# Optimization experiments

Hardware: AMD Instinct MI355X
Metric: run time of the kernel (lower is better)

## Reference

```python
import jax, jax.numpy as jnp
import numpy as np

L, B, CIN, COUT, E, S = 4, 4, 64, 64, 512, 2048
EPS = 1e-6


def setup_inputs() -> dict:
    key = jax.random.key(0)
    ks = jax.random.split(key, 12)
    r = lambda k, shape: (jax.random.normal(k, shape, jnp.float32) * 0.02)
    return {
        'x': jax.random.normal(ks[0], (B, CIN, S), jnp.float32),
        'in_W': r(ks[1], (E, CIN)), 'in_b': jnp.zeros((E,), jnp.float32),
        'cc_W': r(ks[2], (E, E, 3)), 'cc_b': jnp.zeros((E,), jnp.float32),
        'ln1_g': jnp.ones((L, E), jnp.float32), 'ln1_b': jnp.zeros((L, E), jnp.float32),
        'ln2_g': jnp.ones((L, E), jnp.float32), 'ln2_b': jnp.zeros((L, E), jnp.float32),
        'Wq': r(ks[3], (L, E, E)), 'bq': jnp.zeros((L, E), jnp.float32),
        'Wk': r(ks[4], (L, E, E)), 'bk': jnp.zeros((L, E), jnp.float32),
        'Wv': r(ks[5], (L, E, E)), 'bv': jnp.zeros((L, E), jnp.float32),
        'Wo': r(ks[6], (L, E, E)), 'bo': jnp.zeros((L, E), jnp.float32),
        'c1_W': r(ks[7], (L, E, E)), 'c1_b': jnp.zeros((L, E), jnp.float32),
        'c2_W': r(ks[8], (L, E, E)), 'c2_b': jnp.zeros((L, E), jnp.float32),
        'out_W': r(ks[9], (COUT, E)), 'out_b': jnp.zeros((COUT,), jnp.float32),
    }


def _ln(x, g, b):
    m = jnp.mean(x, axis=-1, keepdims=True)
    v = jnp.var(x, axis=-1, keepdims=True)
    return (x - m) * jax.lax.rsqrt(v + 1e-5) * g + b


def _phi(z):
    return jax.nn.elu(z) + 1.0  # linear-attention feature map


def _lin_causal_attn(h, Wq, bq, Wk, bk, Wv, bv, Wo, bo):
    # h: [B, S, E]; causal linear attention in exact masked-quadratic form
    q = _phi(h @ Wq.T + bq)
    k = _phi(h @ Wk.T + bk)
    v = h @ Wv.T + bv
    scores = jnp.einsum('bse,bte->bst', q, k)  # [B, S, S]
    s = h.shape[1]
    mask = jnp.tril(jnp.ones((s, s), bool))
    scores = jnp.where(mask[None], scores, 0.0)
    num = jnp.einsum('bst,bte->bse', scores, v)
    den = jnp.sum(scores, axis=-1, keepdims=True)
    return (num / (den + EPS)) @ Wo.T + bo


def _causal_conv(z, W, b):
    # z: [B, E, S], W: [E, E, 3]; left-pad kernel-1 for causality
    y = jax.lax.conv_general_dilated(z, W, (1,), [(2, 0)],
                                     dimension_numbers=('NCH', 'OIH', 'NCH'))
    return y + b[None, :, None]


def _forward(x, in_W, in_b, cc_W, cc_b, ln1_g, ln1_b, ln2_g, ln2_b,
             Wq, bq, Wk, bk, Wv, bv, Wo, bo, c1_W, c1_b, c2_W, c2_b,
             out_W, out_b):
    lat = jnp.einsum('bcs,ec->bes', x, in_W) + in_b[None, :, None]  # input_layer (k=1 conv)
    lat = _causal_conv(lat, cc_W, cc_b)
    lat = lat.transpose(0, 2, 1)  # [B, S, E]
    for i in range(Wq.shape[0]):
        h = _ln(lat, ln1_g[i], ln1_b[i])
        lat = lat + _lin_causal_attn(h, Wq[i], bq[i], Wk[i], bk[i],
                                     Wv[i], bv[i], Wo[i], bo[i])
        h = _ln(lat, ln2_g[i], ln2_b[i])
        h = jax.nn.gelu(h @ c1_W[i].T + c1_b[i], approximate=False) @ c2_W[i].T + c2_b[i]
        lat = lat + h
    return jnp.einsum('bse,oe->bos', lat, out_W) + out_b[None, :, None]


def reference(x, in_W, in_b, cc_W, cc_b, ln1_g, ln1_b, ln2_g, ln2_b,
              Wq, bq, Wk, bk, Wv, bv, Wo, bo, c1_W, c1_b, c2_W, c2_b,
              out_W, out_b):
    return _forward(x, in_W, in_b, cc_W, cc_b, ln1_g, ln1_b, ln2_g, ln2_b,
                    Wq, bq, Wk, bk, Wv, bv, Wo, bo, c1_W, c1_b, c2_W, c2_b,
                    out_W, out_b)
```

## Files before the change

### kernel.cpp

```cpp
#include <hip/hip_runtime.h>
#include <hip/hip_bf16.h>
#include <cmath>

#define S_LEN 2048
#define E_DIM 512
#define B_SZ 4
#define CIN_D 64
#define COUT_D 64
#define L_NUM 4
#define CHK 256
#define NCHK 8
#define ROWS (B_SZ * S_LEN)
#define PADR 2050
#define QLD 1024

typedef __attribute__((ext_vector_type(8))) short short8;
typedef __attribute__((ext_vector_type(4))) float f32x4;
typedef unsigned short ushort_t;

__device__ __forceinline__ ushort_t f2b(float v) {
  __hip_bfloat16 t = __float2bfloat16(v);
  return __builtin_bit_cast(ushort_t, t);
}
__device__ __forceinline__ float b2f(ushort_t u) {
  return __builtin_bit_cast(float, ((unsigned)u) << 16);
}
__device__ __forceinline__ float b2f(unsigned u) {
  return __builtin_bit_cast(float, u << 16);
}

__device__ __forceinline__ void gload16(const void* g, void* l) {
  __builtin_amdgcn_global_load_lds((const __attribute__((address_space(1))) void*)g,
                                   (__attribute__((address_space(3))) void*)l, 16, 0, 0);
}

__device__ __forceinline__ void barrier_mem() {
  asm volatile("s_barrier" ::: "memory");
}
template <int N>
__device__ __forceinline__ void waitn() {
  if constexpr (N == 0) asm volatile("s_waitcnt vmcnt(0)" ::: "memory");
  else if constexpr (N == 6) asm volatile("s_waitcnt vmcnt(6)" ::: "memory");
  else asm volatile("s_waitcnt vmcnt(8)" ::: "memory");
  __builtin_amdgcn_sched_barrier(0);
}

struct GemmP {
  const ushort_t* A; const ushort_t* B; const float* bias;
  ushort_t* Cb; const float* den;
  int nkt, lda, ldb, ldc;
  int aZrow, aZcol, bZrow, bZcol, cZrow;
  const ushort_t* A2; const ushort_t* B2;
  int nkt2, lda2, ldb2, a2Zrow, b2Zrow;
};

template <int TM, int TN, bool CONV>
__device__ __forceinline__ void mma_phase(const ushort_t* A, const ushort_t* B,
                                          int nkt, int lda, int ldb, int arow0,
                                          int acol0, int brow0, int bcol0,
                                          char* sm, int tid,
                                          f32x4 (&acc)[TM / 32][TN / 32]) {
  constexpr int MF = TM / 32, NF = TN / 32;
  constexpr int ABY = TM * 128, BBY = TN * 128, BUF = ABY + BBY;
  constexpr int RA = ABY / 4096, RB = BBY / 4096;
  const int lane = tid & 63, w = tid >> 6;
  const int wr = (w >> 1) * (TM / 2), wc = (w & 1) * (TN / 2);
  const int l15 = lane & 15, l4 = lane >> 4;

  auto stage = [&](int kt, int buf) {
    int ar0 = arow0, ac0 = acol0 + (kt << 6);
    if (CONV) {
      ar0 = arow0 + (kt >> 3);
      ac0 = acol0 + ((kt & 7) << 6);
    }
    char* s = sm + buf * BUF;
#pragma unroll
    for (int r = 0; r < RA; ++r) {
      const int f = (r << 12) + (tid << 4);
      const int row = f >> 7, sw = ((((f >> 4) & 7)) ^ (row & 7)) << 3;
      gload16(A + (size_t)(ar0 + row) * lda + ac0 + sw, s + f);
    }
    const int bc0 = bcol0 + (kt << 6);
#pragma unroll
    for (int r = 0; r < RB; ++r) {
      const int f = (r << 12) + (tid << 4);
      const int row = f >> 7, sw = ((((f >> 4) & 7)) ^ (row & 7)) << 3;
      gload16(B + (size_t)(brow0 + row) * ldb + bc0 + sw, s + ABY + f);
    }
  };

  stage(0, 0);
  int cur = 0;
  for (int kt = 0; kt < nkt; ++kt) {
    if (kt + 1 < nkt) {
      stage(kt + 1, cur ^ 1);
      waitn<RA + RB>();
    } else {
      waitn<0>();
    }
    barrier_mem();
    char* s = sm + cur * BUF;
#pragma unroll
    for (int kk = 0; kk < 2; ++kk) {
      short8 af[MF], bfv[NF];
#pragma unroll
      for (int m = 0; m < MF; ++m) {
        const int rt = wr + (m << 4) + l15;
        af[m] = *(const short8*)(s + rt * 128 +
                                 (((kk << 6) + (l4 << 4)) ^ ((rt & 7) << 4)));
      }
#pragma unroll
      for (int n = 0; n < NF; ++n) {
        const int rt = wc + (n << 4) + l15;
        bfv[n] = *(const short8*)(s + ABY + rt * 128 +
                                  (((kk << 6) + (l4 << 4)) ^ ((rt & 7) << 4)));
      }
#pragma unroll
      for (int m = 0; m < MF; ++m)
#pragma unroll
        for (int n = 0; n < NF; ++n)
          acc[m][n] = __builtin_amdgcn_mfma_f32_16x16x32_bf16(af[m], bfv[n],
                                                              acc[m][n], 0, 0, 0);
    }
    __builtin_amdgcn_sched_barrier(0);
    asm volatile("s_waitcnt lgkmcnt(0)" ::: "memory");
    barrier_mem();
    cur ^= 1;
  }
}

template <int TM, int TN, int ACT, bool READC, bool PADA, bool PADC,
          bool BIASROW, bool TRIMASK, bool SKIPUP, bool DIVDEN, bool TWOPH,
          bool CONV, bool HALFK>
__device__ __forceinline__ void gemm_body(const GemmP& p, int bm, int bn,
                                          int z, int tid, char* smem) {
  constexpr int MF = TM / 32, NF = TN / 32;
  const int lane = tid & 63, w = tid >> 6;
  const int wr = (w >> 1) * (TM / 2), wc = (w & 1) * (TN / 2);
  const int l15 = lane & 15, l4 = lane >> 4;

  if (SKIPUP && bn >= bm + TM) {
#pragma unroll
    for (int m = 0; m < MF; ++m)
#pragma unroll
      for (int j = 0; j < 4; ++j) {
        const int rloc = bm + wr + (m << 4) + (l4 << 2) + j;
        const size_t crow = (size_t)p.cZrow * z + rloc;
#pragma unroll
        for (int n = 0; n < NF; ++n)
          p.Cb[crow * p.ldc + bn + wc + (n << 4) + l15] = 0;
      }
    return;
  }

  f32x4 acc[MF][NF];
#pragma unroll
  for (int m = 0; m < MF; ++m)
#pragma unroll
    for (int n = 0; n < NF; ++n)
#pragma unroll
      for (int j = 0; j < 4; ++j) acc[m][n][j] = 0.f;

  int arow0 = bm + p.aZrow * z;
  if (PADA) arow0 = bm + ((bm >> 11) << 1);
  int nkt1 = p.nkt;
  if (HALFK) nkt1 = min(p.nkt, (bm + TM) >> 6);
  mma_phase<TM, TN, CONV>(p.A, p.B, nkt1, p.lda, p.ldb, arow0, p.aZcol * z,
                          bn + p.bZrow * z, p.bZcol * z, smem, tid, acc);
  if (TWOPH)
    mma_phase<TM, TN, false>(p.A2, p.B2, p.nkt2, p.lda2, p.ldb2,
                             bm + p.a2Zrow * z, 0, bn + p.b2Zrow * z, 0, smem,
                             tid, acc);

  float bcol[NF];
  if (p.bias && !BIASROW) {
#pragma unroll
    for (int n = 0; n < NF; ++n) bcol[n] = p.bias[bn + wc + (n << 4) + l15];
  }
  int crow_base = bm;
  if (PADC) crow_base = bm + ((bm >> 11) << 1) + 2;
#pragma unroll
  for (int m = 0; m < MF; ++m) {
#pragma unroll
    for (int j = 0; j < 4; ++j) {
      const int rloc = wr + (m << 4) + (l4 << 2) + j;
      const size_t crow = (size_t)p.cZrow * z + crow_base + rloc;
      float inv = 1.f;
      if (DIVDEN) inv = 1.f / (p.den[crow] + 1e-6f);
      float brbias = 0.f;
      if (BIASROW && p.bias) brbias = p.bias[bm + rloc];
#pragma unroll
      for (int n = 0; n < NF; ++n) {
        const int col = bn + wc + (n << 4) + l15;
        float v = acc[m][n][j];
        if (p.bias) v += BIASROW ? brbias : bcol[n];
        if (ACT == 1) v = v > 0.f ? v + 1.f : __expf(v);
        if (ACT == 2) v = 0.5f * v * (1.f + erff(v * 0.70710678118654752f));
        if (ACT == 3 && (bm + rloc) < 512) v = v > 0.f ? v + 1.f : __expf(v);
        if (TRIMASK) {
          if (col > bm + rloc) v = 0.f;
        }
        const size_t cidx = crow * p.ldc + col;
        if (READC) v += b2f(p.Cb[cidx]);
        if (DIVDEN) v *= inv;
        p.Cb[cidx] = f2b(v);
      }
    }
  }
}

__device__ __forceinline__ void swz_decode(int r, int gx, int gy, int swz,
                                           int& bx, int& by) {
  if (swz) {
    const int per = gx * gy, cpx = per >> 3;
    const int s = (r & 7) * cpx + (r >> 3);
    if (gx >= gy) { bx = s / gy; by = s % gy; }
    else          { by = s / gx; bx = s % gx; }
  } else {
    bx = r % gx;
    by = r / gx;
  }
}

template <int TM, int TN, int ACT, bool READC, bool PADA, bool PADC,
          bool BIASROW, bool TRIMASK, bool SKIPUP, bool DIVDEN, bool TWOPH,
          bool CONV, bool SWZ, bool HALFK>
__global__ __launch_bounds__(256) void gemm_mfma(GemmP p) {
  __shared__ __align__(16) char smem[2 * (TM + TN) * 128];
  int bxx = blockIdx.x, byy = blockIdx.y;
  if (SWZ) {
    const int gx = gridDim.x, gy = gridDim.y;
    swz_decode(byy * gx + bxx, gx, gy, 1, bxx, byy);
  }
  gemm_body<TM, TN, ACT, READC, PADA, PADC, BIASROW, TRIMASK, SKIPUP, DIVDEN,
            TWOPH, CONV, HALFK>(p, bxx * TM, byy * TN, blockIdx.z, threadIdx.x,
                                smem);
}


__device__ __forceinline__ void ksum_body(const ushort_t* __restrict__ kT,
                                          float* __restrict__ ks, int unit,
                                          int nunits, int tid) {
  const int wid = tid >> 6, lane = tid & 63;
  const int nw = nunits << 2;
  for (int it = (unit << 2) + wid; it < B_SZ * 7 * E_DIM; it += nw) {
    const int zi = it >> 9, e = it & 511;
    const int z = ((zi / 7) << 3) + zi % 7;
    const uint2 u =
        *(const uint2*)(kT + (size_t)e * ROWS + (z << 8) + (lane << 2));
    float s = b2f(u.x & 0xffffu) + b2f(u.x >> 16) + b2f(u.y & 0xffffu) +
              b2f(u.y >> 16);
#pragma unroll
    for (int off = 32; off; off >>= 1) s += __shfl_xor(s, off);
    if (lane == 0) ks[(z << 9) + e] = s;
  }
}


__global__ __launch_bounds__(256) void mega_qkv(GemmP pa, GemmP pb) {
  __shared__ __align__(16) char smem[65536];
  const int tid = threadIdx.x;
  const int bid = blockIdx.x;
  if (bid < 512) {
    int bx, by;
    swz_decode(bid, 64, 8, 1, bx, by);
    gemm_body<128, 128, 1, 0, 0, 0, 0, 0, 0, 0, 0, 0, 0>(pa, bx << 7, by << 7,
                                                          0, tid, smem);
  } else {
    int bx, by;
    swz_decode(bid - 512, 8, 64, 1, bx, by);
    gemm_body<128, 128, 3, 0, 0, 0, 1, 0, 0, 0, 0, 0, 0>(pb, bx << 7, by << 7,
                                                          0, tid, smem);
  }
}

__global__ __launch_bounds__(256) void mega_psck(GemmP pp, GemmP ps,
                                                 const ushort_t* kT,
                                                 float* ks) {
  __shared__ __align__(16) char smem[65536];
  const int tid = threadIdx.x;
  const int bid = blockIdx.x;
  if (bid < 448) {
    int z = bid >> 4;
    z = (z / 7) * 8 + z % 7;
    const int r = bid & 15;
    gemm_body<128, 128, 0, 0, 0, 0, 0, 0, 0, 0, 0, 0, 0>(
        pp, (r & 3) << 7, (r >> 2) << 7, z, tid, smem);
  } else if (bid < 704) {
    const int v = bid - 448;
    const int z = v >> 3, r = v & 7;
    gemm_body<128, 64, 0, 0, 0, 0, 0, 1, 1, 0, 0, 0, 0>(
        ps, (r & 1) << 7, (r >> 1) << 6, z, tid, smem);
  } else {
    ksum_body(kT, ks, bid - 704, 256, tid);
  }
}


struct CvtP {
  const float *in_W, *cc_W, *Wq, *Wk, *Wv, *Wo, *c1W, *c2W, *bq, *bk, *bv;
  ushort_t *winb, *wconv, *wqkb, *wkvb, *wob, *wc1, *wc2;
  float *bqk, *bkv;
  ushort_t* t2pad;
};
__global__ void cvt_all(CvtP c) {
  const size_t NT = 32768 + 786432 + 2097152 * 2 + 1048576 * 3 + 4096 * 2 + 4096;
  for (size_t i = (size_t)blockIdx.x * 256 + threadIdx.x; i < NT;
       i += (size_t)gridDim.x * 256) {
    size_t j = i;
    if (j < 32768) { c.winb[j] = f2b(c.in_W[j]); continue; }
    j -= 32768;
    if (j < 786432) {
      size_t n = j / 1536, r = j % 1536;
      c.wconv[j] = f2b(c.cc_W[n * 1536 + (r & 511) * 3 + (r >> 9)]);
      continue;
    }
    j -= 786432;
    if (j < 2097152) {
      size_t l = j >> 19, r = j & 524287, row = r >> 9, k = r & 511;
      c.wqkb[j] = f2b(row < 512 ? c.Wq[l * 262144 + row * 512 + k]
                                : c.Wk[l * 262144 + (row - 512) * 512 + k]);
      continue;
    }
    j -= 2097152;
    if (j < 2097152) {
      size_t l = j >> 19, r = j & 524287, row = r >> 9, k = r & 511;
      c.wkvb[j] = f2b(row < 512 ? c.Wk[l * 262144 + row * 512 + k]
                                : c.Wv[l * 262144 + (row - 512) * 512 + k]);
      continue;
    }
    j -= 2097152;
    if (j < 1048576) { c.wob[j] = f2b(c.Wo[j]); continue; }
    j -= 1048576;
    if (j < 1048576) { c.wc1[j] = f2b(c.c1W[j]); continue; }
    j -= 1048576;
    if (j < 1048576) { c.wc2[j] = f2b(c.c2W[j]); continue; }
    j -= 1048576;
    if (j < 4096) {
      size_t l = j >> 10, r = j & 1023;
      c.bqk[j] = r < 512 ? c.bq[l * 512 + r] : c.bk[l * 512 + r - 512];
      continue;
    }
    j -= 4096;
    if (j < 4096) {
      size_t l = j >> 10, r = j & 1023;
      c.bkv[j] = r < 512 ? c.bk[l * 512 + r] : c.bv[l * 512 + r - 512];
      continue;
    }
    j -= 4096;
    {
      int b = (int)(j >> 10), r = (int)(j & 1023);
      c.t2pad[(size_t)(b * PADR) * E_DIM + r] = 0;
    }
  }
}

__global__ __launch_bounds__(256) void transpose_x(const float* __restrict__ x,
                                                   ushort_t* __restrict__ xT) {
  __shared__ float t[64][65];
  const int b = blockIdx.z, s0 = blockIdx.x << 6, tid = threadIdx.x;
#pragma unroll
  for (int i = 0; i < 16; ++i) {
    int idx = tid + (i << 8);
    int c = idx >> 6, s = idx & 63;
    t[c][s] = x[(((size_t)(b * CIN_D + c)) << 11) + s0 + s];
  }
  __syncthreads();
#pragma unroll
  for (int i = 0; i < 16; ++i) {
    int idx = tid + (i << 8);
    int s = idx >> 6, c = idx & 63;
    xT[(((size_t)(b * S_LEN + s0 + s)) << 6) + c] = f2b(t[c][s]);
  }
}

__global__ __launch_bounds__(256) void layernorm_b(const ushort_t* __restrict__ x,
                                                   const float* __restrict__ g,
                                                   const float* __restrict__ bb,
                                                   ushort_t* __restrict__ y) {
  const int wid = threadIdx.x >> 6, lane = threadIdx.x & 63;
  const int row = (blockIdx.x << 2) + wid;
  const ushort_t* xr = x + ((size_t)row << 9);
  const uint4 u = *(const uint4*)(xr + (lane << 3));
  float v[8];
  v[0] = b2f(u.x & 0xffffu); v[1] = b2f(u.x >> 16);
  v[2] = b2f(u.y & 0xffffu); v[3] = b2f(u.y >> 16);
  v[4] = b2f(u.z & 0xffffu); v[5] = b2f(u.z >> 16);
  v[6] = b2f(u.w & 0xffffu); v[7] = b2f(u.w >> 16);
  float s = 0.f, q2 = 0.f;
#pragma unroll
  for (int i = 0; i < 8; ++i) { s += v[i]; q2 += v[i] * v[i]; }
#pragma unroll
  for (int off = 32; off; off >>= 1) {
    s += __shfl_xor(s, off);
    q2 += __shfl_xor(q2, off);
  }
  const float m = s * (1.f / 512.f);
  const float r = rsqrtf(q2 * (1.f / 512.f) - m * m + 1e-5f);
  const int c = lane << 3;
  const float4 g0 = *(const float4*)(g + c);
  const float4 g1 = *(const float4*)(g + c + 4);
  const float4 b0 = *(const float4*)(bb + c);
  const float4 b1 = *(const float4*)(bb + c + 4);
  uint4 o;
  o.x = ((unsigned)f2b((v[1] - m) * r * g0.y + b0.y) << 16) |
        f2b((v[0] - m) * r * g0.x + b0.x);
  o.y = ((unsigned)f2b((v[3] - m) * r * g0.w + b0.w) << 16) |
        f2b((v[2] - m) * r * g0.z + b0.z);
  o.z = ((unsigned)f2b((v[5] - m) * r * g1.y + b1.y) << 16) |
        f2b((v[4] - m) * r * g1.x + b1.x);
  o.w = ((unsigned)f2b((v[7] - m) * r * g1.w + b1.w) << 16) |
        f2b((v[6] - m) * r * g1.z + b1.z);
  *(uint4*)(y + ((size_t)row << 9) + c) = o;
}

__global__ __launch_bounds__(256) void misc_k(
    const ushort_t* __restrict__ Pb, ushort_t* __restrict__ PTb,
    const ushort_t* __restrict__ Sc, const ushort_t* __restrict__ qk,
    const float* __restrict__ ksum, float* __restrict__ den) {
  int bid = blockIdx.x;
  if (bid < 4096) {
    const size_t idx = ((size_t)bid << 8) + threadIdx.x;
    const int b = (int)(idx >> 18);
    const size_t r = idx & ((1u << 18) - 1);
    float acc = 0.f;
#pragma unroll
    for (int j = 0; j < NCHK; ++j) {
      const size_t o = (((size_t)(b * NCHK + j)) << 18) + r;
      PTb[o] = f2b(acc);
      if (j < NCHK - 1) acc += b2f(Pb[o]);
    }
  } else {
    bid -= 4096;
    const int wid = threadIdx.x >> 6, lane = threadIdx.x & 63;
    const int row = (bid << 2) + wid;
    const int z = row >> 8, sl = row & 255;
    const ushort_t* sr = Sc + (((size_t)z) << 16) + ((size_t)sl << 8);
    float s = 0.f;
#pragma unroll
    for (int t = 0; t < 4; ++t) s += b2f(sr[lane + (t << 6)]);
    const ushort_t* qr = qk + (size_t)row * QLD;
    const int j0 = z & ~7;
    for (int e = lane; e < E_DIM; e += 64) {
      float kp = 0.f;
      for (int j = j0; j < z; ++j) kp += ksum[(j << 9) + e];
      s += b2f(qr[e]) * kp;
    }
#pragma unroll
    for (int off = 32; off; off >>= 1) s += __shfl_xor(s, off);
    if (lane == 0) den[row] = s;
  }
}

__global__ __launch_bounds__(256) void out_proj(const ushort_t* __restrict__ lat,
                                                const float* __restrict__ W,
                                                const float* __restrict__ bias,
                                                float* __restrict__ out) {
  const int b = blockIdx.z, bs = blockIdx.x << 6;
  const int tid = threadIdx.x, tm = tid >> 4, tn = tid & 15;
  const int lr = tid >> 2, lc = (tid & 3) << 2;
  __shared__ float As[16][64], Ws[16][64];
  float acc[4][4] = {{0.f}};
  for (int k0 = 0; k0 < E_DIM; k0 += 16) {
    const uint2 ra =
        *(const uint2*)(lat + (((size_t)(b * S_LEN + bs + lr)) << 9) + k0 + lc);
    As[lc + 0][lr] = b2f(ra.x & 0xffffu);
    As[lc + 1][lr] = b2f(ra.x >> 16);
    As[lc + 2][lr] = b2f(ra.y & 0xffffu);
    As[lc + 3][lr] = b2f(ra.y >> 16);
    float4 wv = *(const float4*)(W + (((size_t)lr) << 9) + k0 + lc);
    Ws[lc + 0][lr] = wv.x; Ws[lc + 1][lr] = wv.y;
    Ws[lc + 2][lr] = wv.z; Ws[lc + 3][lr] = wv.w;
    __syncthreads();
#pragma unroll
    for (int kk = 0; kk < 16; ++kk) {
      const float4 a4 = *(const float4*)&As[kk][tm << 2];
      const float4 b4 = *(const float4*)&Ws[kk][tn << 2];
      const float aa[4] = {a4.x, a4.y, a4.z, a4.w};
      const float bb[4] = {b4.x, b4.y, b4.z, b4.w};
#pragma unroll
      for (int i = 0; i < 4; ++i)
#pragma unroll
        for (int j2 = 0; j2 < 4; ++j2) acc[i][j2] += aa[i] * bb[j2];
    }
    __syncthreads();
  }
#pragma unroll
  for (int i = 0; i < 4; ++i)
#pragma unroll
    for (int j2 = 0; j2 < 4; ++j2) {
      const int o = (tn << 2) + j2, sl = bs + (tm << 2) + i;
      out[(((size_t)(b * COUT_D + o)) << 11) + sl] = acc[i][j2] + bias[o];
    }
}

extern "C" void kernel_launch(void* const* d_in, const int* in_sizes, int n_in,
                              void* d_out, int out_size, void* d_ws,
                              size_t ws_size, hipStream_t stream) {
  const float* x = (const float*)d_in[0];
  const float* in_W = (const float*)d_in[1];
  const float* in_b = (const float*)d_in[2];
  const float* cc_W = (const float*)d_in[3];
  const float* cc_b = (const float*)d_in[4];
  const float* ln1g = (const float*)d_in[5];
  const float* ln1b = (const float*)d_in[6];
  const float* ln2g = (const float*)d_in[7];
  const float* ln2b = (const float*)d_in[8];
  const float* Wq = (const float*)d_in[9];
  const float* bq = (const float*)d_in[10];
  const float* Wk = (const float*)d_in[11];
  const float* bk = (const float*)d_in[12];
  const float* Wv = (const float*)d_in[13];
  const float* bv = (const float*)d_in[14];
  const float* Wo = (const float*)d_in[15];
  const float* bo = (const float*)d_in[16];
  const float* c1W = (const float*)d_in[17];
  const float* c1b = (const float*)d_in[18];
  const float* c2W = (const float*)d_in[19];
  const float* c2b = (const float*)d_in[20];
  const float* oW = (const float*)d_in[21];
  const float* ob = (const float*)d_in[22];
  float* out = (float*)d_out;

  const size_t NE = (size_t)ROWS * E_DIM;
  float* ks = (float*)d_ws;
  float* den = ks + 16384;
  float* bqk = den + 8192;
  float* bkv = bqk + 4096;
  ushort_t* u = (ushort_t*)(bkv + 4096);
  ushort_t* latb = u;   u += NE;
  ushort_t* Pb = u;     u += 8388608;
  ushort_t* xT = u;     u += (size_t)ROWS * CIN_D;
  ushort_t* t2pad = u;  u += (size_t)B_SZ * PADR * E_DIM;
  ushort_t* h = u;      u += NE;
  ushort_t* qk = u;     u += (size_t)ROWS * QLD;
  ushort_t* kvT = u;    u += (size_t)1024 * ROWS;
  ushort_t* PTb = u;    u += 8388608;
  ushort_t* t2b = u;    u += NE;
  ushort_t* winb = u;   u += 32768;
  ushort_t* wconv = u;  u += 786432;
  ushort_t* wqkb = u;   u += 2097152;
  ushort_t* wkvb = u;   u += 2097152;
  ushort_t* wob = u;    u += 1048576;
  ushort_t* wc1 = u;    u += 1048576;
  ushort_t* wc2 = u;    u += 1048576;
  ushort_t* Sc = t2pad;
  ushort_t* kT = kvT;
  ushort_t* vT = kvT + (size_t)512 * ROWS;

  const dim3 blk(256);

  CvtP cp{in_W, cc_W, Wq, Wk, Wv, Wo, c1W, c2W, bq, bk, bv,
          winb, wconv, wqkb, wkvb, wob, wc1, wc2, bqk, bkv, t2pad};
  cvt_all<<<dim3(4096), blk, 0, stream>>>(cp);
  transpose_x<<<dim3(S_LEN / 64, 1, B_SZ), blk, 0, stream>>>(x, xT);

  GemmP p;
  auto clr = [&]() {
    p = GemmP{};
    p.lda = E_DIM; p.ldb = E_DIM; p.ldc = E_DIM;
  };

  clr(); p.A = xT; p.B = winb; p.bias = in_b; p.Cb = t2pad;
  p.nkt = 1; p.lda = 64; p.ldb = 64;
  gemm_mfma<128,128,0,0,0,1,0,0,0,0,0,0,1,0><<<dim3(64,4), blk, 0, stream>>>(p);
  clr(); p.A = t2pad; p.B = wconv; p.bias = cc_b; p.Cb = latb;
  p.nkt = 24; p.ldb = 1536;
  gemm_mfma<128,128,0,0,1,0,0,0,0,0,0,1,1,0><<<dim3(64,4), blk, 0, stream>>>(p);

  for (int i = 0; i < L_NUM; ++i) {
    const size_t wOff = (size_t)i * E_DIM * E_DIM;
    const size_t bOff = (size_t)i * E_DIM;
    layernorm_b<<<dim3(ROWS / 4), blk, 0, stream>>>(latb, ln1g + bOff,
                                                    ln1b + bOff, h);
    GemmP pa{}; pa.lda = E_DIM; pa.ldb = E_DIM;
    pa.A = h; pa.B = wqkb + (size_t)i * 524288; pa.bias = bqk + i * 1024;
    pa.Cb = qk; pa.nkt = 8; pa.ldc = QLD;
    GemmP pb{}; pb.lda = E_DIM; pb.ldb = E_DIM;
    pb.A = wkvb + (size_t)i * 524288; pb.B = h; pb.bias = bkv + i * 1024;
    pb.Cb = kvT; pb.nkt = 8; pb.ldc = ROWS;
    mega_qkv<<<dim3(1024), blk, 0, stream>>>(pa, pb);
    GemmP pp{};
    pp.A = vT; pp.B = kT; pp.Cb = Pb; pp.nkt = 4;
    pp.lda = ROWS; pp.ldb = ROWS; pp.ldc = E_DIM;
    pp.aZcol = CHK; pp.bZcol = CHK; pp.cZrow = E_DIM;
    GemmP ps{};
    ps.A = qk; ps.B = qk + 512; ps.Cb = Sc; ps.nkt = 8;
    ps.lda = QLD; ps.ldb = QLD; ps.ldc = CHK;
    ps.aZrow = CHK; ps.bZrow = CHK; ps.cZrow = CHK;
    mega_psck<<<dim3(960), blk, 0, stream>>>(pp, ps, kT, ks);
    misc_k<<<dim3(6144), blk, 0, stream>>>(Pb, PTb, Sc, qk, ks, den);
    clr(); p.A = Sc; p.B = vT; p.Cb = t2b; p.den = den;
    p.nkt = 4; p.lda = CHK; p.ldb = ROWS; p.aZrow = CHK; p.bZcol = CHK;
    p.cZrow = CHK;
    p.A2 = qk; p.B2 = PTb; p.nkt2 = 8; p.lda2 = QLD; p.ldb2 = E_DIM;
    p.a2Zrow = CHK; p.b2Zrow = E_DIM;
    gemm_mfma<64,128,0,0,0,0,0,0,0,1,1,0,0,1><<<dim3(4,4,B_SZ*NCHK), blk, 0, stream>>>(p);
    clr(); p.A = t2b; p.B = wob + wOff; p.bias = bo + bOff; p.Cb = latb;
    p.nkt = 8;
    gemm_mfma<64,128,0,1,0,0,0,0,0,0,0,0,1,0><<<dim3(128,4), blk, 0, stream>>>(p);
    layernorm_b<<<dim3(ROWS / 4), blk, 0, stream>>>(latb, ln2g + bOff,
                                                    ln2b + bOff, h);
    clr(); p.A = h; p.B = wc1 + wOff; p.bias = c1b + bOff; p.Cb = t2b;
    p.nkt = 8;
    gemm_mfma<64,128,2,0,0,0,0,0,0,0,0,0,1,0><<<dim3(128,4), blk, 0, stream>>>(p);
    clr(); p.A = t2b; p.B = wc2 + wOff; p.bias = c2b + bOff; p.Cb = latb;
    p.nkt = 8;
    gemm_mfma<64,128,0,1,0,0,0,0,0,0,0,0,1,0><<<dim3(128,4), blk, 0, stream>>>(p);
  }
  out_proj<<<dim3(S_LEN / 64, 1, B_SZ), blk, 0, stream>>>(latb, oW, ob, out);
}
```

Measured before the change: 644.0 us.

## Fold LayerNorm into GEMM epilogues using per-row partial statistics

Removes the two standalone LayerNorm kernels per layer. Producer GEMMs now emit per-row partial sums and sums of squares over 64-column slots. Consumer GEMMs read the raw residual stream and apply the normalisation algebraically in the epilogue, with gamma folded into the weights and precomputed per-column correction (W·g) and bias (W·b + bias) terms. This saves a full read and write of the activation tensor twice per layer. In exchange it uses the E[x²]−m² variance form on bf16-rounded values and changes the weight rounding, which may reduce numerical accuracy.

New measurement: 719.1 us. 1.12x slower.

```diff
diff --git a/kernel.cpp b/kernel.cpp
--- a/kernel.cpp
+++ b/kernel.cpp
@@ -52,6 +52,7 @@
   int aZrow, aZcol, bZrow, bZcol, cZrow;
   const ushort_t* A2; const ushort_t* B2;
   int nkt2, lda2, ldb2, a2Zrow, b2Zrow;
+  const float* sin_; float* sout_; const float* cg; const float* dv;
 };
 
 template <int TM, int TN, bool CONV>
@@ -131,7 +132,7 @@
 
 template <int TM, int TN, int ACT, bool READC, bool PADA, bool PADC,
           bool BIASROW, bool TRIMASK, bool SKIPUP, bool DIVDEN, bool TWOPH,
-          bool CONV, bool HALFK>
+          bool CONV, bool HALFK, int LNM, bool SOUT>
 __device__ __forceinline__ void gemm_body(const GemmP& p, int bm, int bn,
                                           int z, int tid, char* smem) {
   constexpr int MF = TM / 32, NF = TN / 32;
@@ -177,6 +178,24 @@
 #pragma unroll
     for (int n = 0; n < NF; ++n) bcol[n] = p.bias[bn + wc + (n << 4) + l15];
   }
+  float rn[NF], rmn[NF];
+  if (LNM == 2) {
+#pragma unroll
+    for (int n = 0; n < NF; ++n) {
+      const int col = bn + wc + (n << 4) + l15;
+      const float* sp_ = p.sin_ + ((size_t)col << 4);
+      float S = 0.f, Q = 0.f;
+#pragma unroll
+      for (int t = 0; t < 4; ++t) {
+        const float4 s4 = *(const float4*)(sp_ + (t << 2));
+        S += s4.x + s4.z;
+        Q += s4.y + s4.w;
+      }
+      const float mm = S * (1.f / 512.f);
+      rn[n] = rsqrtf(Q * (1.f / 512.f) - mm * mm + 1e-5f);
+      rmn[n] = rn[n] * mm;
+    }
+  }
   int crow_base = bm;
   if (PADC) crow_base = bm + ((bm >> 11) << 1) + 2;
 #pragma unroll
@@ -189,11 +208,33 @@
       if (DIVDEN) inv = 1.f / (p.den[crow] + 1e-6f);
       float brbias = 0.f;
       if (BIASROW && p.bias) brbias = p.bias[bm + rloc];
+      float r_ = 1.f, rm_ = 0.f;
+      if (LNM == 1) {
+        const float* sp_ = p.sin_ + (crow << 4);
+        float S = 0.f, Q = 0.f;
+#pragma unroll
+        for (int t = 0; t < 4; ++t) {
+          const float4 s4 = *(const float4*)(sp_ + (t << 2));
+          S += s4.x + s4.z;
+          Q += s4.y + s4.w;
+        }
+        const float mm = S * (1.f / 512.f);
+        r_ = rsqrtf(Q * (1.f / 512.f) - mm * mm + 1e-5f);
+        rm_ = r_ * mm;
+      }
+      float cgr = 0.f, dvr = 0.f;
+      if (LNM == 2) {
+        cgr = p.cg[bm + rloc];
+        dvr = p.dv[bm + rloc];
+      }
+      float sp = 0.f, qp = 0.f;
 #pragma unroll
       for (int n = 0; n < NF; ++n) {
         const int col = bn + wc + (n << 4) + l15;
         float v = acc[m][n][j];
-        if (p.bias) v += BIASROW ? brbias : bcol[n];
+        if (LNM == 1) v = r_ * v - rm_ * p.cg[col] + p.dv[col];
+        else if (LNM == 2) v = rn[n] * v - rmn[n] * cgr + dvr;
+        else if (p.bias) v += BIASROW ? brbias : bcol[n];
         if (ACT == 1) v = v > 0.f ? v + 1.f : __expf(v);
         if (ACT == 2) v = 0.5f * v * (1.f + erff(v * 0.70710678118654752f));
         if (ACT == 3 && (bm + rloc) < 512) v = v > 0.f ? v + 1.f : __expf(v);
@@ -203,7 +244,26 @@
         const size_t cidx = crow * p.ldc + col;
         if (READC) v += b2f(p.Cb[cidx]);
         if (DIVDEN) v *= inv;
-        p.Cb[cidx] = f2b(v);
+        const ushort_t uv = f2b(v);
+        p.Cb[cidx] = uv;
+        if (SOUT) {
+          const float vv = b2f(uv);
+          sp += vv;
+          qp += vv * vv;
+        }
+      }
+      if (SOUT) {
+#pragma unroll
+        for (int off = 1; off < 16; off <<= 1) {
+          sp += __shfl_xor(sp, off);
+          qp += __shfl_xor(qp, off);
+        }
+        if (l15 == 0) {
+          const int slot = (bn + wc) >> 6;
+          float* so = p.sout_ + (crow << 4) + (slot << 1);
+          so[0] = sp;
+          so[1] = qp;
+        }
       }
     }
   }
@@ -224,7 +284,7 @@
 
 template <int TM, int TN, int ACT, bool READC, bool PADA, bool PADC,
           bool BIASROW, bool TRIMASK, bool SKIPUP, bool DIVDEN, bool TWOPH,
-          bool CONV, bool SWZ, bool HALFK>
+          bool CONV, bool SWZ, bool HALFK, int LNM, bool SOUT>
 __global__ __launch_bounds__(256) void gemm_mfma(GemmP p) {
   __shared__ __align__(16) char smem[2 * (TM + TN) * 128];
   int bxx = blockIdx.x, byy = blockIdx.y;
@@ -233,8 +293,8 @@
     swz_decode(byy * gx + bxx, gx, gy, 1, bxx, byy);
   }
   gemm_body<TM, TN, ACT, READC, PADA, PADC, BIASROW, TRIMASK, SKIPUP, DIVDEN,
-            TWOPH, CONV, HALFK>(p, bxx * TM, byy * TN, blockIdx.z, threadIdx.x,
-                                smem);
+            TWOPH, CONV, HALFK, LNM, SOUT>(p, bxx * TM, byy * TN, blockIdx.z,
+                                           threadIdx.x, smem);
 }
 
 
@@ -264,13 +324,13 @@
   if (bid < 512) {
     int bx, by;
     swz_decode(bid, 64, 8, 1, bx, by);
-    gemm_body<128, 128, 1, 0, 0, 0, 0, 0, 0, 0, 0, 0, 0>(pa, bx << 7, by << 7,
-                                                          0, tid, smem);
+    gemm_body<128, 128, 1, 0, 0, 0, 0, 0, 0, 0, 0, 0, 0, 1, 0>(
+        pa, bx << 7, by << 7, 0, tid, smem);
   } else {
     int bx, by;
     swz_decode(bid - 512, 8, 64, 1, bx, by);
-    gemm_body<128, 128, 3, 0, 0, 0, 1, 0, 0, 0, 0, 0, 0>(pb, bx << 7, by << 7,
-                                                          0, tid, smem);
+    gemm_body<128, 128, 3, 0, 0, 0, 0, 0, 0, 0, 0, 0, 0, 2, 0>(
+        pb, bx << 7, by << 7, 0, tid, smem);
   }
 }
 
@@ -284,12 +344,12 @@
     int z = bid >> 4;
     z = (z / 7) * 8 + z % 7;
     const int r = bid & 15;
-    gemm_body<128, 128, 0, 0, 0, 0, 0, 0, 0, 0, 0, 0, 0>(
+    gemm_body<128, 128, 0, 0, 0, 0, 0, 0, 0, 0, 0, 0, 0, 0, 0>(
         pp, (r & 3) << 7, (r >> 2) << 7, z, tid, smem);
   } else if (bid < 704) {
     const int v = bid - 448;
     const int z = v >> 3, r = v & 7;
-    gemm_body<128, 64, 0, 0, 0, 0, 0, 1, 1, 0, 0, 0, 0>(
+    gemm_body<128, 64, 0, 0, 0, 0, 0, 1, 1, 0, 0, 0, 0, 0, 0>(
         ps, (r & 1) << 7, (r >> 1) << 6, z, tid, smem);
   } else {
     ksum_body(kT, ks, bid - 704, 256, tid);
@@ -298,13 +358,16 @@
 
 
 struct CvtP {
-  const float *in_W, *cc_W, *Wq, *Wk, *Wv, *Wo, *c1W, *c2W, *bq, *bk, *bv;
+  const float *in_W, *cc_W, *Wq, *Wk, *Wv, *Wo, *c1W, *c2W;
+  const float *bq, *bk, *bv, *c1b;
+  const float *g1, *b1, *g2, *b2;
   ushort_t *winb, *wconv, *wqkb, *wkvb, *wob, *wc1, *wc2;
-  float *bqk, *bkv;
+  float *cgq, *dq, *cgkv, *dkv, *cg1, *d1;
   ushort_t* t2pad;
 };
 __global__ void cvt_all(CvtP c) {
-  const size_t NT = 32768 + 786432 + 2097152 * 2 + 1048576 * 3 + 4096 * 2 + 4096;
+  const size_t NT = 32768 + 786432 + 2097152 + 2097152 + 1048576 + 1048576 +
+                    1048576 + 4096 + 10240;
   for (size_t i = (size_t)blockIdx.x * 256 + threadIdx.x; i < NT;
        i += (size_t)gridDim.x * 256) {
     size_t j = i;
@@ -318,39 +381,74 @@
     j -= 786432;
     if (j < 2097152) {
       size_t l = j >> 19, r = j & 524287, row = r >> 9, k = r & 511;
-      c.wqkb[j] = f2b(row < 512 ? c.Wq[l * 262144 + row * 512 + k]
-                                : c.Wk[l * 262144 + (row - 512) * 512 + k]);
+      float wv = row < 512 ? c.Wq[l * 262144 + row * 512 + k]
+                           : c.Wk[l * 262144 + (row - 512) * 512 + k];
+      c.wqkb[j] = f2b(wv * c.g1[l * 512 + k]);
       continue;
     }
     j -= 2097152;
     if (j < 2097152) {
       size_t l = j >> 19, r = j & 524287, row = r >> 9, k = r & 511;
-      c.wkvb[j] = f2b(row < 512 ? c.Wk[l * 262144 + row * 512 + k]
-                                : c.Wv[l * 262144 + (row - 512) * 512 + k]);
+      float wv = row < 512 ? c.Wk[l * 262144 + row * 512 + k]
+                           : c.Wv[l * 262144 + (row - 512) * 512 + k];
+      c.wkvb[j] = f2b(wv * c.g1[l * 512 + k]);
       continue;
     }
     j -= 2097152;
     if (j < 1048576) { c.wob[j] = f2b(c.Wo[j]); continue; }
     j -= 1048576;
-    if (j < 1048576) { c.wc1[j] = f2b(c.c1W[j]); continue; }
+    if (j < 1048576) {
+      size_t l = j >> 18, k = j & 511;
+      c.wc1[j] = f2b(c.c1W[j] * c.g2[l * 512 + k]);
+      continue;
+    }
     j -= 1048576;
     if (j < 1048576) { c.wc2[j] = f2b(c.c2W[j]); continue; }
     j -= 1048576;
     if (j < 4096) {
-      size_t l = j >> 10, r = j & 1023;
-      c.bqk[j] = r < 512 ? c.bq[l * 512 + r] : c.bk[l * 512 + r - 512];
-      continue;
-    }
-    j -= 4096;
-    if (j < 4096) {
-      size_t l = j >> 10, r = j & 1023;
-      c.bkv[j] = r < 512 ? c.bk[l * 512 + r] : c.bv[l * 512 + r - 512];
+      int b = (int)(j >> 10), r = (int)(j & 1023);
+      c.t2pad[(size_t)(b * PADR) * E_DIM + r] = 0;
       continue;
     }
     j -= 4096;
     {
-      int b = (int)(j >> 10), r = (int)(j & 1023);
-      c.t2pad[(size_t)(b * PADR) * E_DIM + r] = 0;
+      const int unit = (int)j;
+      const float *wrow, *gv, *bbv;
+      float *cgp, *dvp;
+      float bias;
+      if (unit < 4096) {
+        const int l = unit >> 10, n = unit & 1023;
+        wrow = n < 512 ? c.Wq + (size_t)l * 262144 + (size_t)n * 512
+                       : c.Wk + (size_t)l * 262144 + (size_t)(n - 512) * 512;
+        gv = c.g1 + l * 512; bbv = c.b1 + l * 512;
+        bias = n < 512 ? c.bq[l * 512 + n] : c.bk[l * 512 + n - 512];
+        cgp = c.cgq + unit; dvp = c.dq + unit;
+      } else if (unit < 8192) {
+        const int u2 = unit - 4096;
+        const int l = u2 >> 10, n = u2 & 1023;
+        wrow = n < 512 ? c.Wk + (size_t)l * 262144 + (size_t)n * 512
+                       : c.Wv + (size_t)l * 262144 + (size_t)(n - 512) * 512;
+        gv = c.g1 + l * 512; bbv = c.b1 + l * 512;
+        bias = n < 512 ? c.bk[l * 512 + n] : c.bv[l * 512 + n - 512];
+        cgp = c.cgkv + u2; dvp = c.dkv + u2;
+      } else {
+        const int u2 = unit - 8192;
+        const int l = u2 >> 9, n = u2 & 511;
+        wrow = c.c1W + (size_t)l * 262144 + (size_t)n * 512;
+        gv = c.g2 + l * 512; bbv = c.b2 + l * 512;
+        bias = c.c1b[l * 512 + n];
+        cgp = c.cg1 + u2; dvp = c.d1 + u2;
+      }
+      float s1 = 0.f, s2 = 0.f;
+      for (int k = 0; k < 512; k += 4) {
+        const float4 w4 = *(const float4*)(wrow + k);
+        const float4 g4 = *(const float4*)(gv + k);
+        const float4 b4 = *(const float4*)(bbv + k);
+        s1 += w4.x * g4.x + w4.y * g4.y + w4.z * g4.z + w4.w * g4.w;
+        s2 += w4.x * b4.x + w4.y * b4.y + w4.z * b4.z + w4.w * b4.w;
+      }
+      *cgp = s1;
+      *dvp = s2 + bias;
     }
   }
 }
@@ -372,46 +470,6 @@
     int s = idx >> 6, c = idx & 63;
     xT[(((size_t)(b * S_LEN + s0 + s)) << 6) + c] = f2b(t[c][s]);
   }
-}
-
-__global__ __launch_bounds__(256) void layernorm_b(const ushort_t* __restrict__ x,
-                                                   const float* __restrict__ g,
-                                                   const float* __restrict__ bb,
-                                                   ushort_t* __restrict__ y) {
-  const int wid = threadIdx.x >> 6, lane = threadIdx.x & 63;
-  const int row = (blockIdx.x << 2) + wid;
-  const ushort_t* xr = x + ((size_t)row << 9);
-  const uint4 u = *(const uint4*)(xr + (lane << 3));
-  float v[8];
-  v[0] = b2f(u.x & 0xffffu); v[1] = b2f(u.x >> 16);
-  v[2] = b2f(u.y & 0xffffu); v[3] = b2f(u.y >> 16);
-  v[4] = b2f(u.z & 0xffffu); v[5] = b2f(u.z >> 16);
-  v[6] = b2f(u.w & 0xffffu); v[7] = b2f(u.w >> 16);
-  float s = 0.f, q2 = 0.f;
-#pragma unroll
-  for (int i = 0; i < 8; ++i) { s += v[i]; q2 += v[i] * v[i]; }
-#pragma unroll
-  for (int off = 32; off; off >>= 1) {
-    s += __shfl_xor(s, off);
-    q2 += __shfl_xor(q2, off);
-  }
-  const float m = s * (1.f / 512.f);
-  const float r = rsqrtf(q2 * (1.f / 512.f) - m * m + 1e-5f);
-  const int c = lane << 3;
-  const float4 g0 = *(const float4*)(g + c);
-  const float4 g1 = *(const float4*)(g + c + 4);
-  const float4 b0 = *(const float4*)(bb + c);
-  const float4 b1 = *(const float4*)(bb + c + 4);
-  uint4 o;
-  o.x = ((unsigned)f2b((v[1] - m) * r * g0.y + b0.y) << 16) |
-        f2b((v[0] - m) * r * g0.x + b0.x);
-  o.y = ((unsigned)f2b((v[3] - m) * r * g0.w + b0.w) << 16) |
-        f2b((v[2] - m) * r * g0.z + b0.z);
-  o.z = ((unsigned)f2b((v[5] - m) * r * g1.y + b1.y) << 16) |
-        f2b((v[4] - m) * r * g1.x + b1.x);
-  o.w = ((unsigned)f2b((v[7] - m) * r * g1.w + b1.w) << 16) |
-        f2b((v[6] - m) * r * g1.z + b1.z);
-  *(uint4*)(y + ((size_t)row << 9) + c) = o;
 }
 
 __global__ __launch_bounds__(256) void misc_k(
@@ -525,14 +583,19 @@
   const size_t NE = (size_t)ROWS * E_DIM;
   float* ks = (float*)d_ws;
   float* den = ks + 16384;
-  float* bqk = den + 8192;
-  float* bkv = bqk + 4096;
-  ushort_t* u = (ushort_t*)(bkv + 4096);
+  float* stats1 = den + 8192;
+  float* stats2 = stats1 + 131072;
+  float* cgq = stats2 + 131072;
+  float* dq = cgq + 4096;
+  float* cgkv = dq + 4096;
+  float* dkv = cgkv + 4096;
+  float* cg1 = dkv + 4096;
+  float* d1 = cg1 + 2048;
+  ushort_t* u = (ushort_t*)(d1 + 2048);
   ushort_t* latb = u;   u += NE;
   ushort_t* Pb = u;     u += 8388608;
   ushort_t* xT = u;     u += (size_t)ROWS * CIN_D;
   ushort_t* t2pad = u;  u += (size_t)B_SZ * PADR * E_DIM;
-  ushort_t* h = u;      u += NE;
   ushort_t* qk = u;     u += (size_t)ROWS * QLD;
   ushort_t* kvT = u;    u += (size_t)1024 * ROWS;
   ushort_t* PTb = u;    u += 8388608;
@@ -550,8 +613,10 @@
 
   const dim3 blk(256);
 
-  CvtP cp{in_W, cc_W, Wq, Wk, Wv, Wo, c1W, c2W, bq, bk, bv,
-          winb, wconv, wqkb, wkvb, wob, wc1, wc2, bqk, bkv, t2pad};
+  CvtP cp{in_W, cc_W, Wq, Wk, Wv, Wo, c1W, c2W, bq, bk, bv, c1b,
+          ln1g, ln1b, ln2g, ln2b,
+          winb, wconv, wqkb, wkvb, wob, wc1, wc2,
+          cgq, dq, cgkv, dkv, cg1, d1, t2pad};
   cvt_all<<<dim3(4096), blk, 0, stream>>>(cp);
   transpose_x<<<dim3(S_LEN / 64, 1, B_SZ), blk, 0, stream>>>(x, xT);
 
@@ -563,22 +628,22 @@
 
   clr(); p.A = xT; p.B = winb; p.bias = in_b; p.Cb = t2pad;
   p.nkt = 1; p.lda = 64; p.ldb = 64;
-  gemm_mfma<128,128,0,0,0,1,0,0,0,0,0,0,1,0><<<dim3(64,4), blk, 0, stream>>>(p);
+  gemm_mfma<128,128,0,0,0,1,0,0,0,0,0,0,1,0,0,0><<<dim3(64,4), blk, 0, stream>>>(p);
   clr(); p.A = t2pad; p.B = wconv; p.bias = cc_b; p.Cb = latb;
-  p.nkt = 24; p.ldb = 1536;
-  gemm_mfma<128,128,0,0,1,0,0,0,0,0,0,1,1,0><<<dim3(64,4), blk, 0, stream>>>(p);
+  p.nkt = 24; p.ldb = 1536; p.sout_ = stats1;
+  gemm_mfma<128,128,0,0,1,0,0,0,0,0,0,1,1,0,0,1><<<dim3(64,4), blk, 0, stream>>>(p);
 
   for (int i = 0; i < L_NUM; ++i) {
     const size_t wOff = (size_t)i * E_DIM * E_DIM;
     const size_t bOff = (size_t)i * E_DIM;
-    layernorm_b<<<dim3(ROWS / 4), blk, 0, stream>>>(latb, ln1g + bOff,
-                                                    ln1b + bOff, h);
     GemmP pa{}; pa.lda = E_DIM; pa.ldb = E_DIM;
-    pa.A = h; pa.B = wqkb + (size_t)i * 524288; pa.bias = bqk + i * 1024;
+    pa.A = latb; pa.B = wqkb + (size_t)i * 524288;
     pa.Cb = qk; pa.nkt = 8; pa.ldc = QLD;
+    pa.sin_ = stats1; pa.cg = cgq + i * 1024; pa.dv = dq + i * 1024;
     GemmP pb{}; pb.lda = E_DIM; pb.ldb = E_DIM;
-    pb.A = wkvb + (size_t)i * 524288; pb.B = h; pb.bias = bkv + i * 1024;
+    pb.A = wkvb + (size_t)i * 524288; pb.B = latb;
     pb.Cb = kvT; pb.nkt = 8; pb.ldc = ROWS;
+    pb.sin_ = stats1; pb.cg = cgkv + i * 1024; pb.dv = dkv + i * 1024;
     mega_qkv<<<dim3(1024), blk, 0, stream>>>(pa, pb);
     GemmP pp{};
     pp.A = vT; pp.B = kT; pp.Cb = Pb; pp.nkt = 4;
@@ -595,18 +660,16 @@
     p.cZrow = CHK;
     p.A2 = qk; p.B2 = PTb; p.nkt2 = 8; p.lda2 = QLD; p.ldb2 = E_DIM;
     p.a2Zrow = CHK; p.b2Zrow = E_DIM;
-    gemm_mfma<64,128,0,0,0,0,0,0,0,1,1,0,0,1><<<dim3(4,4,B_SZ*NCHK), blk, 0, stream>>>(p);
+    gemm_mfma<64,128,0,0,0,0,0,0,0,1,1,0,0,1,0,0><<<dim3(4,4,B_SZ*NCHK), blk, 0, stream>>>(p);
     clr(); p.A = t2b; p.B = wob + wOff; p.bias = bo + bOff; p.Cb = latb;
-    p.nkt = 8;
-    gemm_mfma<64,128,0,1,0,0,0,0,0,0,0,0,1,0><<<dim3(128,4), blk, 0, stream>>>(p);
-    layernorm_b<<<dim3(ROWS / 4), blk, 0, stream>>>(latb, ln2g + bOff,
-                                                    ln2b + bOff, h);
-    clr(); p.A = h; p.B = wc1 + wOff; p.bias = c1b + bOff; p.Cb = t2b;
-    p.nkt = 8;
-    gemm_mfma<64,128,2,0,0,0,0,0,0,0,0,0,1,0><<<dim3(128,4), blk, 0, stream>>>(p);
+    p.nkt = 8; p.sout_ = stats2;
+    gemm_mfma<64,128,0,1,0,0,0,0,0,0,0,0,1,0,0,1><<<dim3(128,4), blk, 0, stream>>>(p);
+    clr(); p.A = latb; p.B = wc1 + wOff; p.Cb = t2b; p.nkt = 8;
+    p.sin_ = stats2; p.cg = cg1 + i * 512; p.dv = d1 + i * 512;
+    gemm_mfma<64,128,2,0,0,0,0,0,0,0,0,0,1,0,1,0><<<dim3(128,4), blk, 0, stream>>>(p);
     clr(); p.A = t2b; p.B = wc2 + wOff; p.bias = c2b + bOff; p.Cb = latb;
-    p.nkt = 8;
-    gemm_mfma<64,128,0,1,0,0,0,0,0,0,0,0,1,0><<<dim3(128,4), blk, 0, stream>>>(p);
+    p.nkt = 8; p.sout_ = stats1;
+    gemm_mfma<64,128,0,1,0,0,0,0,0,0,0,0,1,0,0,1><<<dim3(128,4), blk, 0, stream>>>(p);
   }
   out_proj<<<dim3(S_LEN / 64, 1, B_SZ), blk, 0, stream>>>(latb, oW, ob, out);
 }
```
